# Kernel optimization log

Hardware: AMD Instinct MI355X
Metric: run time of the kernel (lower is better)

Reference implementation:

```python
import jax, jax.numpy as jnp
import numpy as np

ALPHA = 0.7
GAMMA = 0.2
INF = 1e9


def setup_inputs() -> dict:
    key = jax.random.key(0)
    k1, k2 = jax.random.split(key)
    B, T, C = 64, 1024, 8
    pred = jax.random.normal(k1, (B, T, C), dtype=jnp.float32)
    target = jax.random.normal(k2, (B, T, C), dtype=jnp.float32)
    return {"pred": pred, "target": target}


def _soft_dtw(pred, target, gamma):
    # pred, target: [B, T, C]; squared-Euclidean pairwise cost D: [B, T, T]
    B, T, _ = pred.shape
    x2 = jnp.sum(pred * pred, axis=-1)          # [B, T]
    y2 = jnp.sum(target * target, axis=-1)      # [B, T]
    D = x2[:, :, None] + y2[:, None, :] - 2.0 * jnp.einsum('btc,bsc->bts', pred, target)

    i_idx = jnp.arange(T)

    def step(carry, k):
        # anti-diagonal wavefront: diagonal k holds cells (i, k-i)
        r_km2, r_km1 = carry                     # each [B, T], indexed by row i
        j_idx = k - i_idx
        valid = (j_idx >= 0) & (j_idx < T)
        jc = jnp.clip(j_idx, 0, T - 1)
        d_k = D[:, i_idx, jc]                    # [B, T]
        # neighbors: R[i-1, j] and R[i, j-1] on diag k-1; R[i-1, j-1] on diag k-2
        up = jnp.concatenate([jnp.full((B, 1), INF, D.dtype), r_km1[:, :-1]], axis=1)
        left = r_km1
        diag = jnp.concatenate([jnp.full((B, 1), INF, D.dtype), r_km2[:, :-1]], axis=1)
        # virtual origin R[-1,-1] = 0 feeds cell (0,0) on diagonal k == 0
        diag = jnp.where(((k == 0) & (i_idx == 0))[None, :], 0.0, diag)
        stacked = jnp.stack([up, left, diag], axis=0)          # [3, B, T]
        smin = -gamma * jax.nn.logsumexp(-stacked / gamma, axis=0)
        r_new = jnp.where(valid[None, :], d_k + smin, INF)
        return (r_km1, r_new), None

    init = (jnp.full((B, T), INF, D.dtype), jnp.full((B, T), INF, D.dtype))
    (_, r_last), _ = jax.lax.scan(step, init, jnp.arange(2 * T - 1))
    # R[T-1, T-1] sits on the last diagonal at row index T-1
    return jnp.mean(r_last[:, T - 1])


def reference(pred, target):
    mse = jnp.mean((pred - target) ** 2)
    sdtw = _soft_dtw(pred, target, GAMMA)
    return ALPHA * mse + (1.0 - ALPHA) * sdtw
```

## Files before the change

kernel.cpp:

```cpp
#include <hip/hip_runtime.h>


constexpr int TT = 1024;
constexpr float ALPHA_ = 0.7f;
constexpr float FINF = 1000000000.0f;
constexpr int RING = 1088;

__device__ __forceinline__ float shflup1(float old0, float v) {
    return __int_as_float(__builtin_amdgcn_update_dpp(
        __float_as_int(old0), __float_as_int(v), 0x138, 0xf, 0xf, false));
}
__device__ __forceinline__ float rotdn1(float v) {
    return __int_as_float(__builtin_amdgcn_update_dpp(
        0, __float_as_int(v), 0x130, 0xf, 0xf, false));
}

__global__ __launch_bounds__(256) void sdtw_band_kernel(
    const float* __restrict__ pred, const float* __restrict__ target,
    float* __restrict__ ws)
{
    __shared__ float4 s_c4[TT * 3];
    __shared__ float  s_row[4][1088];
    __shared__ float  s_red[4];
    __shared__ int    s_prog[4];

    const int blk = blockIdx.x;
    const int b   = blk & 63;
    const int q   = blk >> 6;
    const int tid = threadIdx.x;
    const int l   = tid & 63;
    const int w_  = __builtin_amdgcn_readfirstlane(tid >> 6);
    const int g   = (q << 2) + w_;
    const int gbase = g << 6;
    const int row   = gbase + l;

    if (tid < 4) s_prog[tid] = -1;

    const float* pr = pred   + ((size_t)b * TT + row) * 8;
    const float* tr = target + ((size_t)b * TT + row) * 8;
    const float4 pa = ((const float4*)pr)[0];
    const float4 pb = ((const float4*)pr)[1];
    const float4 ma = ((const float4*)tr)[0];
    const float4 mb = ((const float4*)tr)[1];

    float x2 = 0.f, msep = 0.f;
    {
        const float pp[8] = {pa.x,pa.y,pa.z,pa.w,pb.x,pb.y,pb.z,pb.w};
        const float tt[8] = {ma.x,ma.y,ma.z,ma.w,mb.x,mb.y,mb.z,mb.w};
        #pragma unroll
        for (int c = 0; c < 8; ++c) {
            x2 = fmaf(pp[c], pp[c], x2);
            float d = pp[c] - tt[c];
            msep = fmaf(d, d, msep);
        }
    }
    const float* tg = target + (size_t)b * TT * 8;
    #pragma unroll
    for (int c0 = 0; c0 < 4; ++c0) {
        const int col = tid + (c0 << 8);
        const float4 u0 = ((const float4*)(tg + (size_t)col * 8))[0];
        const float4 u1 = ((const float4*)(tg + (size_t)col * 8))[1];
        const float y2 = u0.x*u0.x + u0.y*u0.y + u0.z*u0.z + u0.w*u0.w
                       + u1.x*u1.x + u1.y*u1.y + u1.z*u1.z + u1.w*u1.w;
        s_c4[3*col]   = make_float4(-2.f*u0.x, -2.f*u0.y, -2.f*u0.z, -2.f*u0.w);
        s_c4[3*col+1] = make_float4(-2.f*u1.x, -2.f*u1.y, -2.f*u1.z, -2.f*u1.w);
        s_c4[3*col+2] = make_float4(y2, 0.f, 0.f, 0.f);
    }
    #pragma unroll
    for (int off = 32; off > 0; off >>= 1) msep += __shfl_down(msep, off, 64);
    if (l == 0) s_red[w_] = msep;
    __syncthreads();
    if (tid == 0) ws[blk] = s_red[0] + s_red[1] + s_red[2] + s_red[3];

    unsigned long long* rings = (unsigned long long*)(ws + 320);
    unsigned long long* pub = rings + (size_t)(q * 64 + b) * RING;
    unsigned long long* con = rings + (size_t)((q - 1) * 64 + b) * RING;
    const int kb_pub   = 256 * q + 192;
    const int kb_con   = 256 * q - 64;
    const int kmax_con = kb_con + 1086;

    const float c1 = 7.213475204444817f;
    const float c2 = 0.13862943611198906f;
    const int amin = g << 2;
    const int amax = amin + 67;
    const int prodmax = amin + 63;

    float r1 = FINF, r2 = FINF;
    unsigned long long pe1 = 0, pe2 = 0;
    int ppf = 0;
    float hpf1 = 0.f, hpf2 = 0.f;
    int hpff = 0;
    float hv, hvd;

    auto stage_halo = [&](int a, int k0, int u) {
        if (w_ == 0) {
            if (q == 0) {
                hv  = FINF;
                hvd = (u == 0 && l == 0) ? 0.0f : FINF;
            } else {
                const int kk1 = k0 - 1 + l, kk2 = k0 - 2 + l;
                const int id1 = min(kk1 - kb_con, RING - 1);
                const int id2 = min(kk2 - kb_con, RING - 1);
                const bool n1 = (l < 16) && (kk1 <= kmax_con);
                const bool n2 = (l < 16) && (kk2 <= kmax_con);
                unsigned long long e1, e2;
                if (ppf) { e1 = pe1; e2 = pe2; ppf = 0; }
                else {
                    e1 = __hip_atomic_load(con + id1, __ATOMIC_RELAXED,
                                           __HIP_MEMORY_SCOPE_AGENT);
                    e2 = __hip_atomic_load(con + id2, __ATOMIC_RELAXED,
                                           __HIP_MEMORY_SCOPE_AGENT);
                }
                while (!__all(((!n1) | ((int)(e1 >> 32) == kk1)) &
                              ((!n2) | ((int)(e2 >> 32) == kk2)))) {
                    e1 = __hip_atomic_load(con + id1, __ATOMIC_RELAXED,
                                           __HIP_MEMORY_SCOPE_AGENT);
                    e2 = __hip_atomic_load(con + id2, __ATOMIC_RELAXED,
                                           __HIP_MEMORY_SCOPE_AGENT);
                }
                hv  = n1 ? __uint_as_float((unsigned)e1) : FINF;
                hvd = n2 ? __uint_as_float((unsigned)e2) : FINF;
            }
        } else {
            if (hpff) { hv = hpf1; hvd = hpf2; hpff = 0; }
            else {
                const int need = (a < prodmax) ? a : prodmax;
                int pv;
                do {
                    pv = __hip_atomic_load(&s_prog[w_ - 1], __ATOMIC_ACQUIRE,
                                           __HIP_MEMORY_SCOPE_WORKGROUP);
                } while (pv < need);
                const int bi = (u << 4) + 63 + l;
                hv  = s_row[w_ - 1][min(bi,     1087)];
                hvd = s_row[w_ - 1][min(bi - 1, 1087)];
            }
        }
    };

#define DFAST(i, DST) do {                                                  \
        const int j_  = jb1 + (i);                                          \
        const float4 va_ = s_c4[3*j_];                                      \
        const float4 vb_ = s_c4[3*j_+1];                                    \
        const float  yv_ = s_c4[3*j_+2].x;                                  \
        float ac_ = x2 + yv_, ac2_ = 0.f;                                   \
        ac_  = fmaf(pa.x, va_.x, ac_ );  ac2_ = fmaf(pa.y, va_.y, ac2_);    \
        ac_  = fmaf(pa.z, va_.z, ac_ );  ac2_ = fmaf(pa.w, va_.w, ac2_);    \
        ac_  = fmaf(pb.x, vb_.x, ac_ );  ac2_ = fmaf(pb.y, vb_.y, ac2_);    \
        ac_  = fmaf(pb.z, vb_.z, ac_ );  ac2_ = fmaf(pb.w, vb_.w, ac2_);    \
        DST = ac_ + ac2_;                                                   \
    } while (0)

#define DCLAMP(JB, i, DST) do {                                             \
        int jc_ = (JB) + (i);                                               \
        jc_ = jc_ < 0 ? 0 : (jc_ > (TT-1) ? (TT-1) : jc_);                  \
        const float4 va_ = s_c4[3*jc_];                                     \
        const float4 vb_ = s_c4[3*jc_+1];                                   \
        const float  yv_ = s_c4[3*jc_+2].x;                                 \
        float ac_ = x2 + yv_, ac2_ = 0.f;                                   \
        ac_  = fmaf(pa.x, va_.x, ac_ );  ac2_ = fmaf(pa.y, va_.y, ac2_);    \
        ac_  = fmaf(pa.z, va_.z, ac_ );  ac2_ = fmaf(pa.w, va_.w, ac2_);    \
        ac_  = fmaf(pb.x, vb_.x, ac_ );  ac2_ = fmaf(pb.y, vb_.y, ac2_);    \
        ac_  = fmaf(pb.z, vb_.z, ac_ );  ac2_ = fmaf(pb.w, vb_.w, ac2_);    \
        DST = ac_ + ac2_;                                                   \
    } while (0)

#define RSTEP(i, DIN, RH, MASKED) do {                                      \
        const float up_   = shflup1(hv,  r1);                               \
        const float dgv_  = shflup1(hvd, r2);                               \
        const float left_ = r1;                                             \
        hv = rotdn1(hv); hvd = rotdn1(hvd);                                 \
        float m_, M_;                                                       \
        asm("v_min3_f32 %0, %1, %2, %3"                                     \
            : "=v"(m_) : "v"(up_), "v"(left_), "v"(dgv_));                  \
        asm("v_max3_f32 %0, %1, %2, %3"                                     \
            : "=v"(M_) : "v"(up_), "v"(left_), "v"(dgv_));                  \
        const float md_ = __builtin_amdgcn_fmed3f(up_, left_, dgv_);        \
        const float mc_ = m_ * c1;                                          \
        const float ea_ = __builtin_amdgcn_exp2f(fmaf(md_, -c1, mc_));      \
        const float eb_ = __builtin_amdgcn_exp2f(fmaf(M_,  -c1, mc_));      \
        const float lg_ = __builtin_amdgcn_logf(1.0f + (ea_ + eb_));        \
        float rn_ = (DIN) + fmaf(-c2, lg_, m_);                             \
        if (MASKED)                                                         \
            rn_ = ((unsigned)(jb0 + (i)) < (unsigned)TT) ? rn_ : FINF;      \
        r2 = r1; r1 = rn_; RH = rn_;                                        \
    } while (0)

    float Dc0,Dc1,Dc2,Dc3,Dc4,Dc5,Dc6,Dc7;
    float Dc8,Dc9,Dc10,Dc11,Dc12,Dc13,Dc14,Dc15;
    {
        const int jb = -l;
        DCLAMP(jb, 0,Dc0 ); DCLAMP(jb, 1,Dc1 ); DCLAMP(jb, 2,Dc2 );
        DCLAMP(jb, 3,Dc3 ); DCLAMP(jb, 4,Dc4 ); DCLAMP(jb, 5,Dc5 );
        DCLAMP(jb, 6,Dc6 ); DCLAMP(jb, 7,Dc7 ); DCLAMP(jb, 8,Dc8 );
        DCLAMP(jb, 9,Dc9 ); DCLAMP(jb,10,Dc10); DCLAMP(jb,11,Dc11);
        DCLAMP(jb,12,Dc12); DCLAMP(jb,13,Dc13); DCLAMP(jb,14,Dc14);
        DCLAMP(jb,15,Dc15);
    }
    float rh14_last = FINF;

    for (int u = 0; u <= 67; ++u) {
        const int a  = amin + u;
        const int k0 = a << 4;
        const int jb0 = (u << 4) - l;
        const int jb1 = jb0 + 16;

        stage_halo(a, k0, u);

        float E0,E1,E2,E3,E4,E5,E6,E7,E8,E9,E10,E11,E12,E13,E14,E15;
        float rh0,rh1,rh2,rh3,rh4,rh5,rh6,rh7;
        float rh8,rh9,rh10,rh11,rh12,rh13,rh14,rh15;

        if (u >= 4 && u <= 62) {
            RSTEP( 0,Dc0 ,rh0 ,0); DFAST( 0,E0 );
            RSTEP( 1,Dc1 ,rh1 ,0); DFAST( 1,E1 );
            RSTEP( 2,Dc2 ,rh2 ,0); DFAST( 2,E2 );
            RSTEP( 3,Dc3 ,rh3 ,0); DFAST( 3,E3 );
            RSTEP( 4,Dc4 ,rh4 ,0); DFAST( 4,E4 );
            RSTEP( 5,Dc5 ,rh5 ,0); DFAST( 5,E5 );
            RSTEP( 6,Dc6 ,rh6 ,0); DFAST( 6,E6 );
            RSTEP( 7,Dc7 ,rh7 ,0); DFAST( 7,E7 );
            RSTEP( 8,Dc8 ,rh8 ,0); DFAST( 8,E8 );
            RSTEP( 9,Dc9 ,rh9 ,0); DFAST( 9,E9 );
            RSTEP(10,Dc10,rh10,0); DFAST(10,E10);
            RSTEP(11,Dc11,rh11,0); DFAST(11,E11);
            RSTEP(12,Dc12,rh12,0); DFAST(12,E12);
            RSTEP(13,Dc13,rh13,0); DFAST(13,E13);
            RSTEP(14,Dc14,rh14,0); DFAST(14,E14);
            RSTEP(15,Dc15,rh15,0); DFAST(15,E15);
        } else {
            RSTEP( 0,Dc0 ,rh0 ,1); RSTEP( 1,Dc1 ,rh1 ,1);
            RSTEP( 2,Dc2 ,rh2 ,1); RSTEP( 3,Dc3 ,rh3 ,1);
            RSTEP( 4,Dc4 ,rh4 ,1); RSTEP( 5,Dc5 ,rh5 ,1);
            RSTEP( 6,Dc6 ,rh6 ,1); RSTEP( 7,Dc7 ,rh7 ,1);
            RSTEP( 8,Dc8 ,rh8 ,1); RSTEP( 9,Dc9 ,rh9 ,1);
            RSTEP(10,Dc10,rh10,1); RSTEP(11,Dc11,rh11,1);
            RSTEP(12,Dc12,rh12,1); RSTEP(13,Dc13,rh13,1);
            RSTEP(14,Dc14,rh14,1); RSTEP(15,Dc15,rh15,1);
            if (u < 67) {
                DCLAMP(jb1, 0,E0 ); DCLAMP(jb1, 1,E1 ); DCLAMP(jb1, 2,E2 );
                DCLAMP(jb1, 3,E3 ); DCLAMP(jb1, 4,E4 ); DCLAMP(jb1, 5,E5 );
                DCLAMP(jb1, 6,E6 ); DCLAMP(jb1, 7,E7 ); DCLAMP(jb1, 8,E8 );
                DCLAMP(jb1, 9,E9 ); DCLAMP(jb1,10,E10); DCLAMP(jb1,11,E11);
                DCLAMP(jb1,12,E12); DCLAMP(jb1,13,E13); DCLAMP(jb1,14,E14);
                DCLAMP(jb1,15,E15);
            } else {
                E0=E1=E2=E3=E4=E5=E6=E7=0.f;
                E8=E9=E10=E11=E12=E13=E14=E15=0.f;
                rh14_last = rh14;
            }
        }

        if (l == 63) {
            float4* dst = (float4*)&s_row[w_][u << 4];
            dst[0] = make_float4(rh0,  rh1,  rh2,  rh3);
            dst[1] = make_float4(rh4,  rh5,  rh6,  rh7);
            dst[2] = make_float4(rh8,  rh9,  rh10, rh11);
            dst[3] = make_float4(rh12, rh13, rh14, rh15);
        }
        Dc0=E0;  Dc1=E1;  Dc2=E2;  Dc3=E3;  Dc4=E4;  Dc5=E5;  Dc6=E6;  Dc7=E7;
        Dc8=E8;  Dc9=E9;  Dc10=E10;Dc11=E11;Dc12=E12;Dc13=E13;Dc14=E14;Dc15=E15;

        if (w_ < 3 && l == 0) {
            __hip_atomic_store(&s_prog[w_], a, __ATOMIC_RELEASE,
                               __HIP_MEMORY_SCOPE_WORKGROUP);
        }
        if (w_ == 3 && q < 3) {
            if (l < 16) {
                const int kk = k0 + l;
                const unsigned long long ev =
                    ((unsigned long long)(unsigned)kk << 32) |
                    (unsigned long long)__float_as_uint(s_row[3][(u << 4) + l]);
                __hip_atomic_store(pub + (kk - kb_pub), ev,
                                   __ATOMIC_RELAXED, __HIP_MEMORY_SCOPE_AGENT);
            }
        }
        if (w_ == 0 && q > 0 && a < amax) {
            const int k0n = k0 + 16;
            const int kk1 = k0n - 1 + l, kk2 = k0n - 2 + l;
            pe1 = __hip_atomic_load(con + min(kk1 - kb_con, RING - 1),
                                    __ATOMIC_RELAXED, __HIP_MEMORY_SCOPE_AGENT);
            pe2 = __hip_atomic_load(con + min(kk2 - kb_con, RING - 1),
                                    __ATOMIC_RELAXED, __HIP_MEMORY_SCOPE_AGENT);
            ppf = 1;
        }
        if (w_ != 0 && a < amax) {
            const int neednx = ((a + 1) < prodmax) ? (a + 1) : prodmax;
            const int pv = __hip_atomic_load(&s_prog[w_ - 1], __ATOMIC_ACQUIRE,
                                             __HIP_MEMORY_SCOPE_WORKGROUP);
            if (pv >= neednx) {
                const int bi = ((u + 1) << 4) + 63 + l;
                hpf1 = s_row[w_ - 1][min(bi,     1087)];
                hpf2 = s_row[w_ - 1][min(bi - 1, 1087)];
                hpff = 1;
            }
        }
    }
    if (q == 3 && tid == 255) ws[256 + b] = rh14_last;
#undef DFAST
#undef DCLAMP
#undef RSTEP
}

__global__ __launch_bounds__(256) void finalize2_kernel(
    const float* __restrict__ ws, float* __restrict__ out)
{
    __shared__ float sm[4], ss[4];
    const int tid = threadIdx.x, l = tid & 63, w = tid >> 6;
    float m  = ws[tid];
    float sd = (tid < 64) ? ws[256 + tid] : 0.f;
    #pragma unroll
    for (int off = 32; off > 0; off >>= 1) {
        m  += __shfl_down(m,  off, 64);
        sd += __shfl_down(sd, off, 64);
    }
    if (l == 0) { sm[w] = m; ss[w] = sd; }
    __syncthreads();
    if (tid == 0) {
        float M = sm[0] + sm[1] + sm[2] + sm[3];
        float S = ss[0] + ss[1] + ss[2] + ss[3];
        out[0] = ALPHA_ * (M / 524288.0f) + (1.0f - ALPHA_) * (S / 64.0f);
    }
}

extern "C" void kernel_launch(void* const* d_in, const int* in_sizes, int n_in,
                              void* d_out, int out_size, void* d_ws, size_t ws_size,
                              hipStream_t stream) {
    const float* pred   = (const float*)d_in[0];
    const float* target = (const float*)d_in[1];
    float* ws  = (float*)d_ws;
    float* out = (float*)d_out;

    sdtw_band_kernel<<<256, 256, 0, stream>>>(pred, target, ws);
    finalize2_kernel<<<1, 256, 0, stream>>>(ws, out);
}
```

Before: 314.2 us.

## Reuse up-neighbor as next diagonal, drop second halo stream, software-pipeline D loads

Drops the separate diagonal halo stream (hvd/r2). The diagonal neighbour of each step is taken from the previous step's up value, so only one DPP shift and one rotate are needed per step. Halo loads and prefetches from the ring buffer and shared rows drop from two to one. The D-cost computation in the fast path becomes a three-stage register pipeline, with LDS loads issued two steps ahead and written in place into the Dc registers, removing the E-to-Dc copy. The risk is a subtle correctness dependency on the first-step diagonal initialisation, plus extra register pressure.

```diff
diff --git a/kernel.cpp b/kernel.cpp
--- a/kernel.cpp
+++ b/kernel.cpp
@@ -85,72 +85,117 @@
     const int amax = amin + 67;
     const int prodmax = amin + 63;
 
-    float r1 = FINF, r2 = FINF;
-    unsigned long long pe1 = 0, pe2 = 0;
+    float r1 = FINF;
+    float dgp;
+    unsigned long long pe1 = 0;
     int ppf = 0;
-    float hpf1 = 0.f, hpf2 = 0.f;
+    float hpf1 = 0.f;
     int hpff = 0;
-    float hv, hvd;
-
-    auto stage_halo = [&](int a, int k0, int u) {
+    float hv;
+
+    {
+        float hvd0;
         if (w_ == 0) {
             if (q == 0) {
-                hv  = FINF;
-                hvd = (u == 0 && l == 0) ? 0.0f : FINF;
+                hvd0 = (l == 0) ? 0.0f : FINF;
             } else {
-                const int kk1 = k0 - 1 + l, kk2 = k0 - 2 + l;
-                const int id1 = min(kk1 - kb_con, RING - 1);
+                const int kk2 = (amin << 4) - 2 + l;
                 const int id2 = min(kk2 - kb_con, RING - 1);
-                const bool n1 = (l < 16) && (kk1 <= kmax_con);
                 const bool n2 = (l < 16) && (kk2 <= kmax_con);
-                unsigned long long e1, e2;
-                if (ppf) { e1 = pe1; e2 = pe2; ppf = 0; }
-                else {
-                    e1 = __hip_atomic_load(con + id1, __ATOMIC_RELAXED,
-                                           __HIP_MEMORY_SCOPE_AGENT);
+                unsigned long long e2;
+                do {
                     e2 = __hip_atomic_load(con + id2, __ATOMIC_RELAXED,
                                            __HIP_MEMORY_SCOPE_AGENT);
-                }
-                while (!__all(((!n1) | ((int)(e1 >> 32) == kk1)) &
-                              ((!n2) | ((int)(e2 >> 32) == kk2)))) {
-                    e1 = __hip_atomic_load(con + id1, __ATOMIC_RELAXED,
-                                           __HIP_MEMORY_SCOPE_AGENT);
-                    e2 = __hip_atomic_load(con + id2, __ATOMIC_RELAXED,
-                                           __HIP_MEMORY_SCOPE_AGENT);
-                }
-                hv  = n1 ? __uint_as_float((unsigned)e1) : FINF;
-                hvd = n2 ? __uint_as_float((unsigned)e2) : FINF;
+                } while (!__all((!n2) | ((int)(e2 >> 32) == kk2)));
+                hvd0 = n2 ? __uint_as_float((unsigned)e2) : FINF;
             }
         } else {
-            if (hpff) { hv = hpf1; hvd = hpf2; hpff = 0; }
-            else {
-                const int need = (a < prodmax) ? a : prodmax;
-                int pv;
-                do {
-                    pv = __hip_atomic_load(&s_prog[w_ - 1], __ATOMIC_ACQUIRE,
-                                           __HIP_MEMORY_SCOPE_WORKGROUP);
-                } while (pv < need);
-                const int bi = (u << 4) + 63 + l;
-                hv  = s_row[w_ - 1][min(bi,     1087)];
-                hvd = s_row[w_ - 1][min(bi - 1, 1087)];
-            }
-        }
-    };
-
-#define DFAST(i, DST) do {                                                  \
-        const int j_  = jb1 + (i);                                          \
-        const float4 va_ = s_c4[3*j_];                                      \
-        const float4 vb_ = s_c4[3*j_+1];                                    \
-        const float  yv_ = s_c4[3*j_+2].x;                                  \
-        float ac_ = x2 + yv_, ac2_ = 0.f;                                   \
-        ac_  = fmaf(pa.x, va_.x, ac_ );  ac2_ = fmaf(pa.y, va_.y, ac2_);    \
-        ac_  = fmaf(pa.z, va_.z, ac_ );  ac2_ = fmaf(pa.w, va_.w, ac2_);    \
-        ac_  = fmaf(pb.x, vb_.x, ac_ );  ac2_ = fmaf(pb.y, vb_.y, ac2_);    \
-        ac_  = fmaf(pb.z, vb_.z, ac_ );  ac2_ = fmaf(pb.w, vb_.w, ac2_);    \
-        DST = ac_ + ac2_;                                                   \
-    } while (0)
-
-#define DCLAMP(JB, i, DST) do {                                             \
+            const int need0 = (amin < prodmax) ? amin : prodmax;
+            int pv;
+            do {
+                pv = __hip_atomic_load(&s_prog[w_ - 1], __ATOMIC_ACQUIRE,
+                                       __HIP_MEMORY_SCOPE_WORKGROUP);
+            } while (pv < need0);
+            hvd0 = s_row[w_ - 1][min(62 + l, 1087)];
+        }
+        dgp = shflup1(hvd0, FINF);
+    }
+
+#define STEPF(i, BA,BB,BY, CA,CB,CY, DCI, DC2, RH) do {                     \
+        const float up_ = shflup1(hv, r1);                                  \
+        hv = rotdn1(hv);                                                    \
+        const int j_ = jb1 + (i);                                           \
+        BA = s_c4[3*j_]; BB = s_c4[3*j_+1]; BY = s_c4[3*j_+2].x;            \
+        float m_, M_;                                                       \
+        asm("v_min3_f32 %0, %1, %2, %3"                                     \
+            : "=v"(m_) : "v"(up_), "v"(r1), "v"(dgp));                      \
+        asm("v_max3_f32 %0, %1, %2, %3"                                     \
+            : "=v"(M_) : "v"(up_), "v"(r1), "v"(dgp));                      \
+        const float md_ = __builtin_amdgcn_fmed3f(up_, r1, dgp);            \
+        dgp = up_;                                                          \
+        const float mc_ = m_ * c1;                                          \
+        const float ea_ = __builtin_amdgcn_exp2f(fmaf(md_, -c1, mc_));      \
+        const float eb_ = __builtin_amdgcn_exp2f(fmaf(M_,  -c1, mc_));      \
+        {   float ac_ = x2 + CY, ac2_ = 0.f;                                \
+            ac_  = fmaf(pa.x, CA.x, ac_ );  ac2_ = fmaf(pa.y, CA.y, ac2_);  \
+            ac_  = fmaf(pa.z, CA.z, ac_ );  ac2_ = fmaf(pa.w, CA.w, ac2_);  \
+            ac_  = fmaf(pb.x, CB.x, ac_ );  ac2_ = fmaf(pb.y, CB.y, ac2_);  \
+            ac_  = fmaf(pb.z, CB.z, ac_ );  ac2_ = fmaf(pb.w, CB.w, ac2_);  \
+            DC2 = ac_ + ac2_; }                                             \
+        const float lg_ = __builtin_amdgcn_logf(1.0f + (ea_ + eb_));        \
+        const float rn_ = (DCI) + fmaf(-c2, lg_, m_);                       \
+        r1 = rn_; RH = rn_;                                                 \
+    } while (0)
+
+#define STEPF0(i, BA,BB,BY, DCI, RH) do {                                   \
+        const float up_ = shflup1(hv, r1);                                  \
+        hv = rotdn1(hv);                                                    \
+        const int j_ = jb1 + (i);                                           \
+        BA = s_c4[3*j_]; BB = s_c4[3*j_+1]; BY = s_c4[3*j_+2].x;            \
+        float m_, M_;                                                       \
+        asm("v_min3_f32 %0, %1, %2, %3"                                     \
+            : "=v"(m_) : "v"(up_), "v"(r1), "v"(dgp));                      \
+        asm("v_max3_f32 %0, %1, %2, %3"                                     \
+            : "=v"(M_) : "v"(up_), "v"(r1), "v"(dgp));                      \
+        const float md_ = __builtin_amdgcn_fmed3f(up_, r1, dgp);            \
+        dgp = up_;                                                          \
+        const float mc_ = m_ * c1;                                          \
+        const float ea_ = __builtin_amdgcn_exp2f(fmaf(md_, -c1, mc_));      \
+        const float eb_ = __builtin_amdgcn_exp2f(fmaf(M_,  -c1, mc_));      \
+        const float lg_ = __builtin_amdgcn_logf(1.0f + (ea_ + eb_));        \
+        const float rn_ = (DCI) + fmaf(-c2, lg_, m_);                       \
+        r1 = rn_; RH = rn_;                                                 \
+    } while (0)
+
+#define DMATHT(CA,CB,CY, DC2) do {                                          \
+        float ac_ = x2 + CY, ac2_ = 0.f;                                    \
+        ac_  = fmaf(pa.x, CA.x, ac_ );  ac2_ = fmaf(pa.y, CA.y, ac2_);      \
+        ac_  = fmaf(pa.z, CA.z, ac_ );  ac2_ = fmaf(pa.w, CA.w, ac2_);      \
+        ac_  = fmaf(pb.x, CB.x, ac_ );  ac2_ = fmaf(pb.y, CB.y, ac2_);      \
+        ac_  = fmaf(pb.z, CB.z, ac_ );  ac2_ = fmaf(pb.w, CB.w, ac2_);      \
+        DC2 = ac_ + ac2_;                                                   \
+    } while (0)
+
+#define STEPE(i, DCI, RH) do {                                              \
+        const float up_ = shflup1(hv, r1);                                  \
+        hv = rotdn1(hv);                                                    \
+        float m_, M_;                                                       \
+        asm("v_min3_f32 %0, %1, %2, %3"                                     \
+            : "=v"(m_) : "v"(up_), "v"(r1), "v"(dgp));                      \
+        asm("v_max3_f32 %0, %1, %2, %3"                                     \
+            : "=v"(M_) : "v"(up_), "v"(r1), "v"(dgp));                      \
+        const float md_ = __builtin_amdgcn_fmed3f(up_, r1, dgp);            \
+        dgp = up_;                                                          \
+        const float mc_ = m_ * c1;                                          \
+        const float ea_ = __builtin_amdgcn_exp2f(fmaf(md_, -c1, mc_));      \
+        const float eb_ = __builtin_amdgcn_exp2f(fmaf(M_,  -c1, mc_));      \
+        const float lg_ = __builtin_amdgcn_logf(1.0f + (ea_ + eb_));        \
+        float rn_ = (DCI) + fmaf(-c2, lg_, m_);                             \
+        rn_ = ((unsigned)(jb0 + (i)) < (unsigned)TT) ? rn_ : FINF;          \
+        r1 = rn_; RH = rn_;                                                 \
+    } while (0)
+
+#define DCLAMP(JB, i, DC) do {                                              \
         int jc_ = (JB) + (i);                                               \
         jc_ = jc_ < 0 ? 0 : (jc_ > (TT-1) ? (TT-1) : jc_);                  \
         const float4 va_ = s_c4[3*jc_];                                     \
@@ -161,28 +206,7 @@
         ac_  = fmaf(pa.z, va_.z, ac_ );  ac2_ = fmaf(pa.w, va_.w, ac2_);    \
         ac_  = fmaf(pb.x, vb_.x, ac_ );  ac2_ = fmaf(pb.y, vb_.y, ac2_);    \
         ac_  = fmaf(pb.z, vb_.z, ac_ );  ac2_ = fmaf(pb.w, vb_.w, ac2_);    \
-        DST = ac_ + ac2_;                                                   \
-    } while (0)
-
-#define RSTEP(i, DIN, RH, MASKED) do {                                      \
-        const float up_   = shflup1(hv,  r1);                               \
-        const float dgv_  = shflup1(hvd, r2);                               \
-        const float left_ = r1;                                             \
-        hv = rotdn1(hv); hvd = rotdn1(hvd);                                 \
-        float m_, M_;                                                       \
-        asm("v_min3_f32 %0, %1, %2, %3"                                     \
-            : "=v"(m_) : "v"(up_), "v"(left_), "v"(dgv_));                  \
-        asm("v_max3_f32 %0, %1, %2, %3"                                     \
-            : "=v"(M_) : "v"(up_), "v"(left_), "v"(dgv_));                  \
-        const float md_ = __builtin_amdgcn_fmed3f(up_, left_, dgv_);        \
-        const float mc_ = m_ * c1;                                          \
-        const float ea_ = __builtin_amdgcn_exp2f(fmaf(md_, -c1, mc_));      \
-        const float eb_ = __builtin_amdgcn_exp2f(fmaf(M_,  -c1, mc_));      \
-        const float lg_ = __builtin_amdgcn_logf(1.0f + (ea_ + eb_));        \
-        float rn_ = (DIN) + fmaf(-c2, lg_, m_);                             \
-        if (MASKED)                                                         \
-            rn_ = ((unsigned)(jb0 + (i)) < (unsigned)TT) ? rn_ : FINF;      \
-        r2 = r1; r1 = rn_; RH = rn_;                                        \
+        DC = ac_ + ac2_;                                                    \
     } while (0)
 
     float Dc0,Dc1,Dc2,Dc3,Dc4,Dc5,Dc6,Dc7;
@@ -197,6 +221,8 @@
         DCLAMP(jb,15,Dc15);
     }
     float rh14_last = FINF;
+    float4 vA0, vB0, vA1, vB1, vA2, vB2;
+    float  yv0, yv1, yv2;
 
     for (int u = 0; u <= 67; ++u) {
         const int a  = amin + u;
@@ -204,48 +230,77 @@
         const int jb0 = (u << 4) - l;
         const int jb1 = jb0 + 16;
 
-        stage_halo(a, k0, u);
-
-        float E0,E1,E2,E3,E4,E5,E6,E7,E8,E9,E10,E11,E12,E13,E14,E15;
+        if (w_ == 0) {
+            if (q == 0) {
+                hv = FINF;
+            } else {
+                const int kk1 = k0 - 1 + l;
+                const int id1 = min(kk1 - kb_con, RING - 1);
+                const bool n1 = (l < 16) && (kk1 <= kmax_con);
+                unsigned long long e1;
+                if (ppf) { e1 = pe1; ppf = 0; }
+                else {
+                    e1 = __hip_atomic_load(con + id1, __ATOMIC_RELAXED,
+                                           __HIP_MEMORY_SCOPE_AGENT);
+                }
+                while (!__all((!n1) | ((int)(e1 >> 32) == kk1))) {
+                    e1 = __hip_atomic_load(con + id1, __ATOMIC_RELAXED,
+                                           __HIP_MEMORY_SCOPE_AGENT);
+                }
+                hv = n1 ? __uint_as_float((unsigned)e1) : FINF;
+            }
+        } else {
+            if (hpff) { hv = hpf1; hpff = 0; }
+            else {
+                const int need = (a < prodmax) ? a : prodmax;
+                int pv;
+                do {
+                    pv = __hip_atomic_load(&s_prog[w_ - 1], __ATOMIC_ACQUIRE,
+                                           __HIP_MEMORY_SCOPE_WORKGROUP);
+                } while (pv < need);
+                hv = s_row[w_ - 1][min((u << 4) + 63 + l, 1087)];
+            }
+        }
+
         float rh0,rh1,rh2,rh3,rh4,rh5,rh6,rh7;
         float rh8,rh9,rh10,rh11,rh12,rh13,rh14,rh15;
 
         if (u >= 4 && u <= 62) {
-            RSTEP( 0,Dc0 ,rh0 ,0); DFAST( 0,E0 );
-            RSTEP( 1,Dc1 ,rh1 ,0); DFAST( 1,E1 );
-            RSTEP( 2,Dc2 ,rh2 ,0); DFAST( 2,E2 );
-            RSTEP( 3,Dc3 ,rh3 ,0); DFAST( 3,E3 );
-            RSTEP( 4,Dc4 ,rh4 ,0); DFAST( 4,E4 );
-            RSTEP( 5,Dc5 ,rh5 ,0); DFAST( 5,E5 );
-            RSTEP( 6,Dc6 ,rh6 ,0); DFAST( 6,E6 );
-            RSTEP( 7,Dc7 ,rh7 ,0); DFAST( 7,E7 );
-            RSTEP( 8,Dc8 ,rh8 ,0); DFAST( 8,E8 );
-            RSTEP( 9,Dc9 ,rh9 ,0); DFAST( 9,E9 );
-            RSTEP(10,Dc10,rh10,0); DFAST(10,E10);
-            RSTEP(11,Dc11,rh11,0); DFAST(11,E11);
-            RSTEP(12,Dc12,rh12,0); DFAST(12,E12);
-            RSTEP(13,Dc13,rh13,0); DFAST(13,E13);
-            RSTEP(14,Dc14,rh14,0); DFAST(14,E14);
-            RSTEP(15,Dc15,rh15,0); DFAST(15,E15);
+            STEPF0( 0, vA0,vB0,yv0,               Dc0 , rh0 );
+            STEPF0( 1, vA1,vB1,yv1,               Dc1 , rh1 );
+            STEPF ( 2, vA2,vB2,yv2, vA0,vB0,yv0,  Dc2 , Dc0 , rh2 );
+            STEPF ( 3, vA0,vB0,yv0, vA1,vB1,yv1,  Dc3 , Dc1 , rh3 );
+            STEPF ( 4, vA1,vB1,yv1, vA2,vB2,yv2,  Dc4 , Dc2 , rh4 );
+            STEPF ( 5, vA2,vB2,yv2, vA0,vB0,yv0,  Dc5 , Dc3 , rh5 );
+            STEPF ( 6, vA0,vB0,yv0, vA1,vB1,yv1,  Dc6 , Dc4 , rh6 );
+            STEPF ( 7, vA1,vB1,yv1, vA2,vB2,yv2,  Dc7 , Dc5 , rh7 );
+            STEPF ( 8, vA2,vB2,yv2, vA0,vB0,yv0,  Dc8 , Dc6 , rh8 );
+            STEPF ( 9, vA0,vB0,yv0, vA1,vB1,yv1,  Dc9 , Dc7 , rh9 );
+            STEPF (10, vA1,vB1,yv1, vA2,vB2,yv2,  Dc10, Dc8 , rh10);
+            STEPF (11, vA2,vB2,yv2, vA0,vB0,yv0,  Dc11, Dc9 , rh11);
+            STEPF (12, vA0,vB0,yv0, vA1,vB1,yv1,  Dc12, Dc10, rh12);
+            STEPF (13, vA1,vB1,yv1, vA2,vB2,yv2,  Dc13, Dc11, rh13);
+            STEPF (14, vA2,vB2,yv2, vA0,vB0,yv0,  Dc14, Dc12, rh14);
+            STEPF (15, vA0,vB0,yv0, vA1,vB1,yv1,  Dc15, Dc13, rh15);
+            DMATHT(vA2,vB2,yv2, Dc14);
+            DMATHT(vA0,vB0,yv0, Dc15);
         } else {
-            RSTEP( 0,Dc0 ,rh0 ,1); RSTEP( 1,Dc1 ,rh1 ,1);
-            RSTEP( 2,Dc2 ,rh2 ,1); RSTEP( 3,Dc3 ,rh3 ,1);
-            RSTEP( 4,Dc4 ,rh4 ,1); RSTEP( 5,Dc5 ,rh5 ,1);
-            RSTEP( 6,Dc6 ,rh6 ,1); RSTEP( 7,Dc7 ,rh7 ,1);
-            RSTEP( 8,Dc8 ,rh8 ,1); RSTEP( 9,Dc9 ,rh9 ,1);
-            RSTEP(10,Dc10,rh10,1); RSTEP(11,Dc11,rh11,1);
-            RSTEP(12,Dc12,rh12,1); RSTEP(13,Dc13,rh13,1);
-            RSTEP(14,Dc14,rh14,1); RSTEP(15,Dc15,rh15,1);
+            STEPE( 0,Dc0 ,rh0 ); STEPE( 1,Dc1 ,rh1 );
+            STEPE( 2,Dc2 ,rh2 ); STEPE( 3,Dc3 ,rh3 );
+            STEPE( 4,Dc4 ,rh4 ); STEPE( 5,Dc5 ,rh5 );
+            STEPE( 6,Dc6 ,rh6 ); STEPE( 7,Dc7 ,rh7 );
+            STEPE( 8,Dc8 ,rh8 ); STEPE( 9,Dc9 ,rh9 );
+            STEPE(10,Dc10,rh10); STEPE(11,Dc11,rh11);
+            STEPE(12,Dc12,rh12); STEPE(13,Dc13,rh13);
+            STEPE(14,Dc14,rh14); STEPE(15,Dc15,rh15);
             if (u < 67) {
-                DCLAMP(jb1, 0,E0 ); DCLAMP(jb1, 1,E1 ); DCLAMP(jb1, 2,E2 );
-                DCLAMP(jb1, 3,E3 ); DCLAMP(jb1, 4,E4 ); DCLAMP(jb1, 5,E5 );
-                DCLAMP(jb1, 6,E6 ); DCLAMP(jb1, 7,E7 ); DCLAMP(jb1, 8,E8 );
-                DCLAMP(jb1, 9,E9 ); DCLAMP(jb1,10,E10); DCLAMP(jb1,11,E11);
-                DCLAMP(jb1,12,E12); DCLAMP(jb1,13,E13); DCLAMP(jb1,14,E14);
-                DCLAMP(jb1,15,E15);
+                DCLAMP(jb1, 0,Dc0 ); DCLAMP(jb1, 1,Dc1 ); DCLAMP(jb1, 2,Dc2 );
+                DCLAMP(jb1, 3,Dc3 ); DCLAMP(jb1, 4,Dc4 ); DCLAMP(jb1, 5,Dc5 );
+                DCLAMP(jb1, 6,Dc6 ); DCLAMP(jb1, 7,Dc7 ); DCLAMP(jb1, 8,Dc8 );
+                DCLAMP(jb1, 9,Dc9 ); DCLAMP(jb1,10,Dc10); DCLAMP(jb1,11,Dc11);
+                DCLAMP(jb1,12,Dc12); DCLAMP(jb1,13,Dc13); DCLAMP(jb1,14,Dc14);
+                DCLAMP(jb1,15,Dc15);
             } else {
-                E0=E1=E2=E3=E4=E5=E6=E7=0.f;
-                E8=E9=E10=E11=E12=E13=E14=E15=0.f;
                 rh14_last = rh14;
             }
         }
@@ -257,8 +312,6 @@
             dst[2] = make_float4(rh8,  rh9,  rh10, rh11);
             dst[3] = make_float4(rh12, rh13, rh14, rh15);
         }
-        Dc0=E0;  Dc1=E1;  Dc2=E2;  Dc3=E3;  Dc4=E4;  Dc5=E5;  Dc6=E6;  Dc7=E7;
-        Dc8=E8;  Dc9=E9;  Dc10=E10;Dc11=E11;Dc12=E12;Dc13=E13;Dc14=E14;Dc15=E15;
 
         if (w_ < 3 && l == 0) {
             __hip_atomic_store(&s_prog[w_], a, __ATOMIC_RELEASE,
@@ -275,11 +328,8 @@
             }
         }
         if (w_ == 0 && q > 0 && a < amax) {
-            const int k0n = k0 + 16;
-            const int kk1 = k0n - 1 + l, kk2 = k0n - 2 + l;
+            const int kk1 = k0 + 15 + l;
             pe1 = __hip_atomic_load(con + min(kk1 - kb_con, RING - 1),
-                                    __ATOMIC_RELAXED, __HIP_MEMORY_SCOPE_AGENT);
-            pe2 = __hip_atomic_load(con + min(kk2 - kb_con, RING - 1),
                                     __ATOMIC_RELAXED, __HIP_MEMORY_SCOPE_AGENT);
             ppf = 1;
         }
@@ -288,17 +338,17 @@
             const int pv = __hip_atomic_load(&s_prog[w_ - 1], __ATOMIC_ACQUIRE,
                                              __HIP_MEMORY_SCOPE_WORKGROUP);
             if (pv >= neednx) {
-                const int bi = ((u + 1) << 4) + 63 + l;
-                hpf1 = s_row[w_ - 1][min(bi,     1087)];
-                hpf2 = s_row[w_ - 1][min(bi - 1, 1087)];
+                hpf1 = s_row[w_ - 1][min(((u + 1) << 4) + 63 + l, 1087)];
                 hpff = 1;
             }
         }
     }
     if (q == 3 && tid == 255) ws[256 + b] = rh14_last;
-#undef DFAST
+#undef STEPF
+#undef STEPF0
+#undef DMATHT
+#undef STEPE
 #undef DCLAMP
-#undef RSTEP
 }
 
 __global__ __launch_bounds__(256) void finalize2_kernel(
```

After: 306.9 us (median of 2 runs). -2.3%, faster.
